# Kernel tuning notes

Measured on AMD Instinct MI355X. Metric: run time of the kernel, lower is better.

The kernel has to match this reference:

```python
import jax, jax.numpy as jnp
import numpy as np

D = 4
KERNEL = (3, 3, 3, 3)
CIN = 8
COUT = 16
SPATIAL = (24, 24, 24, 24)
B = 8


def setup_inputs() -> dict:
    key = jax.random.key(0)
    k1, k2, k3 = jax.random.split(key, 3)
    x = jax.random.normal(k1, (B, CIN) + SPATIAL, dtype=jnp.float32)
    kmul = int(np.prod(KERNEL))  # 81
    # torch layout: zeros(O, kmul, 1).repeat(1,1,Cin).reshape(O, kmul*Cin)
    # -> flat dim is kernel-major, channel-minor
    weight = jax.random.normal(k2, (COUT, kmul * CIN), dtype=jnp.float32) * 0.05
    bias = jax.random.normal(k3, (COUT,), dtype=jnp.float32) * 0.05
    return {"x": x, "weight": weight, "bias": bias}


def reference(x, weight, bias):
    # Unflatten weight to (O, k1, k2, k3, k4, Cin) matching the unfold's
    # (kernel..., channel) flatten order, then run a direct 4-D 'same' conv
    # (cross-correlation, identical math to the unfold+matmul original).
    w = weight.reshape((COUT,) + KERNEL + (CIN,))
    dn = jax.lax.ConvDimensionNumbers(
        lhs_spec=(0, 1, 2, 3, 4, 5),   # N, C, s1..s4
        rhs_spec=(0, 5, 1, 2, 3, 4),   # O, I, k1..k4  (I lives at axis 5 of w)
        out_spec=(0, 1, 2, 3, 4, 5),   # N, O, s1..s4
    )
    out = jax.lax.conv_general_dilated(
        x, w,
        window_strides=(1,) * D,
        padding=[(1, 1)] * D,
        dimension_numbers=dn,
    )
    return out + bias.reshape((1, COUT) + (1,) * D)
```

## Files before the change

### kernel.cpp

```cpp
#include <hip/hip_runtime.h>
#include <hip/hip_bf16.h>


#define SDIM  24
#define SP    (SDIM * SDIM * SDIM * SDIM)
#define CIN   8
#define COUT  16
#define BATCH 8
#define KW    648
#define NCHUNK 21
#define NB    4
#define PTILES (SP / 16)
#define NBLOCKS ((BATCH / NB) * PTILES / 4)
#define NXCD  8
#define CPX   (NBLOCKS / NXCD)

#define ZERO_OFF 0
#define WPK_OFF  256
#define XT_OFF   32768
#define XT_BYTES ((size_t)BATCH * SP * CIN * 2)
#define WS_NEEDED (XT_OFF + XT_BYTES)

typedef __attribute__((ext_vector_type(8))) short short8;
typedef __attribute__((ext_vector_type(4))) float f32x4;

static __device__ __forceinline__ unsigned short f2bf(float f) {
    unsigned u = __builtin_bit_cast(unsigned, f);
    u = (u + 0x7fffu + ((u >> 16) & 1u)) >> 16;
    return (unsigned short)u;
}

__global__ __launch_bounds__(256) void pack_weights(
    const float* __restrict__ w, unsigned char* __restrict__ ws)
{
    int t = blockIdx.x * 256 + threadIdx.x;
    if (t == 1344) {
        short8 z = {0,0,0,0,0,0,0,0};
        *(short8*)(ws + ZERO_OFF) = z;
    }
    if (t >= NCHUNK * 64) return;
    int chunk = t >> 6;
    int lane  = t & 63;
    int m     = lane & 15;
    int quad  = lane >> 4;
    short8 pk;
    #pragma unroll
    for (int j = 0; j < 8; ++j) {
        int k = chunk * 32 + quad * 8 + j;
        float f = (k < KW) ? w[m * KW + k] : 0.0f;
        pk[j] = (short)f2bf(f);
    }
    ((short8*)(ws + WPK_OFF))[chunk * 64 + lane] = pk;
}

__global__ __launch_bounds__(256) void transpose_x(
    const float* __restrict__ x, unsigned char* __restrict__ ws)
{
    int idx = blockIdx.x * 256 + threadIdx.x;
    int b  = idx / (SP / 2);
    int pp = idx - b * (SP / 2);
    int p  = pp * 2;
    const float* xb = x + (size_t)b * CIN * SP + p;

    float2 v[CIN];
    #pragma unroll
    for (int c = 0; c < CIN; ++c)
        v[c] = *(const float2*)(xb + (size_t)c * SP);

    union { __hip_bfloat162 h2[4]; short8 s8; } u0, u1;
    #pragma unroll
    for (int i = 0; i < 4; ++i) {
        float2 a = make_float2(v[2 * i].x, v[2 * i + 1].x);
        float2 bq = make_float2(v[2 * i].y, v[2 * i + 1].y);
        u0.h2[i] = __float22bfloat162_rn(a);
        u1.h2[i] = __float22bfloat162_rn(bq);
    }
    short8* dst = (short8*)(ws + XT_OFF) + ((size_t)b * SP + p);
    dst[0] = u0.s8;
    dst[1] = u1.s8;
}

__global__ __launch_bounds__(256) void conv4d_mfma(
    const unsigned char* __restrict__ ws,
    const float* __restrict__ bias,
    float* __restrict__ out)
{
    const int lane = threadIdx.x & 63;
    const int wave = threadIdx.x >> 6;
    const int col  = lane & 15;
    const int quad = lane >> 4;

    int bid = blockIdx.x;
    bid = (bid & (NXCD - 1)) * CPX + (bid >> 3);

    int W = bid * 4 + wave;
    W = __builtin_amdgcn_readfirstlane(W);
    const int pt = W % PTILES;
    const int g  = W / PTILES;

    const int p = pt * 16 + col;
    int r = p;
    const int p4 = r % SDIM; r /= SDIM;
    const int p3 = r % SDIM; r /= SDIM;
    const int p2 = r % SDIM;
    const int p1 = r / SDIM;

    const short8* wpk  = (const short8*)(ws + WPK_OFF);
    const short8* xT   = (const short8*)(ws + XT_OFF);
    const short8* zslt = (const short8*)(ws + ZERO_OFF);

    const short8* xb[NB];
    #pragma unroll
    for (int t = 0; t < NB; ++t)
        xb[t] = xT + (size_t)(g * NB + t) * SP;

    f32x4 acc[NB];
    #pragma unroll
    for (int t = 0; t < NB; ++t) acc[t] = (f32x4){0.f, 0.f, 0.f, 0.f};

    #pragma unroll
    for (int c = 0; c < NCHUNK; ++c) {
        short8 afrag = wpk[c * 64 + lane];

        int tap = c * 4 + quad;
        int k1 = tap / 27; int rem = tap - k1 * 27;
        int k2 = rem / 9;  rem -= k2 * 9;
        int k3 = rem / 3;
        int k4 = rem - k3 * 3;
        int q1 = p1 + k1 - 1, q2 = p2 + k2 - 1, q3 = p3 + k3 - 1, q4 = p4 + k4 - 1;
        bool valid = ((unsigned)q1 < (unsigned)SDIM) & ((unsigned)q2 < (unsigned)SDIM) &
                     ((unsigned)q3 < (unsigned)SDIM) & ((unsigned)q4 < (unsigned)SDIM);
        int q = ((q1 * SDIM + q2) * SDIM + q3) * SDIM + q4;

        short8 bf[NB];
        #pragma unroll
        for (int t = 0; t < NB; ++t) {
            const short8* src = valid ? (xb[t] + q) : zslt;
            bf[t] = *src;
        }
        #pragma unroll
        for (int t = 0; t < NB; ++t)
            acc[t] = __builtin_amdgcn_mfma_f32_16x16x32_bf16(afrag, bf[t], acc[t], 0, 0, 0);
    }

    f32x4 b4 = *(const f32x4*)(bias + quad * 4);
    #pragma unroll
    for (int t = 0; t < NB; ++t) {
        float* obase = out + ((size_t)(g * NB + t) * COUT + quad * 4) * SP + p;
        #pragma unroll
        for (int reg = 0; reg < 4; ++reg)
            obase[(size_t)reg * SP] = acc[t][reg] + b4[reg];
    }
}

__global__ __launch_bounds__(256) void conv4d_direct(
    const float* __restrict__ x, const float* __restrict__ w,
    const float* __restrict__ bias, float* __restrict__ out)
{
    int t = blockIdx.x * blockDim.x + threadIdx.x;
    int b = t / SP;
    int p = t - b * SP;
    int p4 = p % SDIM; int tmp = p / SDIM;
    int p3 = tmp % SDIM; tmp /= SDIM;
    int p2 = tmp % SDIM; int p1 = tmp / SDIM;
    float acc[COUT];
    #pragma unroll
    for (int o = 0; o < COUT; ++o) acc[o] = bias[o];
    const float* xb = x + (size_t)b * CIN * SP;
    for (int k1 = 0; k1 < 3; ++k1) {
        unsigned q1 = (unsigned)(p1 + k1 - 1); if (q1 >= SDIM) continue;
        for (int k2 = 0; k2 < 3; ++k2) {
            unsigned q2 = (unsigned)(p2 + k2 - 1); if (q2 >= SDIM) continue;
            for (int k3 = 0; k3 < 3; ++k3) {
                unsigned q3 = (unsigned)(p3 + k3 - 1); if (q3 >= SDIM) continue;
                int base123 = (((int)q1 * SDIM + (int)q2) * SDIM + (int)q3) * SDIM;
                int kf = ((k1 * 3 + k2) * 3 + k3) * 3;
                for (int k4 = 0; k4 < 3; ++k4) {
                    unsigned q4 = (unsigned)(p4 + k4 - 1); if (q4 >= SDIM) continue;
                    int q = base123 + (int)q4;
                    float xv[CIN];
                    #pragma unroll
                    for (int c = 0; c < CIN; ++c) xv[c] = xb[c * SP + q];
                    const float* wp = w + (kf + k4) * CIN;
                    #pragma unroll
                    for (int o = 0; o < COUT; ++o)
                        #pragma unroll
                        for (int c = 0; c < CIN; ++c)
                            acc[o] = fmaf(xv[c], wp[o * KW + c], acc[o]);
                }
            }
        }
    }
    float* ob = out + (size_t)b * COUT * SP + p;
    #pragma unroll
    for (int o = 0; o < COUT; ++o) ob[o * SP] = acc[o];
}

extern "C" void kernel_launch(void* const* d_in, const int* in_sizes, int n_in,
                              void* d_out, int out_size, void* d_ws, size_t ws_size,
                              hipStream_t stream)
{
    const float* x    = (const float*)d_in[0];
    const float* w    = (const float*)d_in[1];
    const float* bias = (const float*)d_in[2];
    float* out        = (float*)d_out;

    if (ws_size < WS_NEEDED) {
        const int total = BATCH * SP;
        hipLaunchKernelGGL(conv4d_direct, dim3(total / 256), dim3(256), 0, stream,
                           x, w, bias, out);
        return;
    }

    unsigned char* ws = (unsigned char*)d_ws;

    hipLaunchKernelGGL(pack_weights, dim3(6), dim3(256), 0, stream, w, ws);

    const int pair_total = BATCH * SP / 2;
    hipLaunchKernelGGL(transpose_x, dim3(pair_total / 256), dim3(256), 0, stream, x, ws);

    hipLaunchKernelGGL(conv4d_mfma, dim3(NBLOCKS), dim3(256), 0, stream,
                       (const unsigned char*)ws, bias, out);
}
```

Measured before the change: 366.8 us.

## Use zero-padded bf16 input layout to remove boundary checks in conv

```diff
diff --git a/kernel.cpp b/kernel.cpp
--- a/kernel.cpp
+++ b/kernel.cpp
@@ -4,6 +4,8 @@
 
 #define SDIM  24
 #define SP    (SDIM * SDIM * SDIM * SDIM)
+#define PD    26
+#define SPPAD (PD * PD * PD * PD)
 #define CIN   8
 #define COUT  16
 #define BATCH 8
@@ -12,14 +14,17 @@
 #define NB    4
 #define PTILES (SP / 16)
 #define NBLOCKS ((BATCH / NB) * PTILES / 4)
-#define NXCD  8
-#define CPX   (NBLOCKS / NXCD)
 
 #define ZERO_OFF 0
 #define WPK_OFF  256
 #define XT_OFF   32768
-#define XT_BYTES ((size_t)BATCH * SP * CIN * 2)
-#define WS_NEEDED (XT_OFF + XT_BYTES)
+#define XT_BYTES  ((size_t)BATCH * SP * CIN * 2)
+#define XTP_BYTES ((size_t)BATCH * SPPAD * CIN * 2)
+#define WS_NEEDED_OLD (XT_OFF + XT_BYTES)
+#define WS_NEEDED_PAD (XT_OFF + XTP_BYTES)
+
+#define ZTOTAL ((size_t)BATCH * SPPAD)
+#define ZBLOCKS 14281
 
 typedef __attribute__((ext_vector_type(8))) short short8;
 typedef __attribute__((ext_vector_type(4))) float f32x4;
@@ -30,14 +35,18 @@
     return (unsigned short)u;
 }
 
-__global__ __launch_bounds__(256) void pack_weights(
+__global__ __launch_bounds__(256) void prep0_pad(
     const float* __restrict__ w, unsigned char* __restrict__ ws)
 {
-    int t = blockIdx.x * 256 + threadIdx.x;
-    if (t == 1344) {
-        short8 z = {0,0,0,0,0,0,0,0};
-        *(short8*)(ws + ZERO_OFF) = z;
-    }
+    if (blockIdx.x < ZBLOCKS) {
+        size_t i = (size_t)blockIdx.x * 256 + threadIdx.x;
+        if (i < ZTOTAL) {
+            short8 z = {0, 0, 0, 0, 0, 0, 0, 0};
+            ((short8*)(ws + XT_OFF))[i] = z;
+        }
+        return;
+    }
+    int t = (blockIdx.x - ZBLOCKS) * 256 + threadIdx.x;
     if (t >= NCHUNK * 64) return;
     int chunk = t >> 6;
     int lane  = t & 63;
@@ -53,6 +62,138 @@
     ((short8*)(ws + WPK_OFF))[chunk * 64 + lane] = pk;
 }
 
+__global__ __launch_bounds__(256) void transpose_xp(
+    const float* __restrict__ x, unsigned char* __restrict__ ws)
+{
+    int idx = blockIdx.x * 256 + threadIdx.x;
+    int b  = idx / (SP / 4);
+    int pq = idx - b * (SP / 4);
+    int p  = pq * 4;
+    const float* xb = x + (size_t)b * CIN * SP + p;
+
+    float4 v[CIN];
+    #pragma unroll
+    for (int c = 0; c < CIN; ++c)
+        v[c] = *(const float4*)(xb + (size_t)c * SP);
+
+    union { __hip_bfloat162 h2[4]; short8 s8; } u[4];
+    #pragma unroll
+    for (int j = 0; j < 4; ++j) {
+        #pragma unroll
+        for (int i = 0; i < 4; ++i) {
+            float a0 = (&v[2 * i].x)[j];
+            float a1 = (&v[2 * i + 1].x)[j];
+            u[j].h2[i] = __float22bfloat162_rn(make_float2(a0, a1));
+        }
+    }
+
+    int r = p;
+    const int p4 = r % SDIM; r /= SDIM;
+    const int p3 = r % SDIM; r /= SDIM;
+    const int p2 = r % SDIM;
+    const int p1 = r / SDIM;
+    int qp = (((p1 + 1) * PD + (p2 + 1)) * PD + (p3 + 1)) * PD + (p4 + 1);
+
+    short8* dst = (short8*)(ws + XT_OFF) + (size_t)b * SPPAD + qp;
+    #pragma unroll
+    for (int j = 0; j < 4; ++j) dst[j] = u[j].s8;
+}
+
+__global__ __launch_bounds__(256) void conv4d_mfma_pad(
+    const unsigned char* __restrict__ ws,
+    const float* __restrict__ bias,
+    float* __restrict__ out)
+{
+    __shared__ int    s_delta[96];
+    __shared__ short8 s_w[NCHUNK * 64];
+
+    const int tid  = threadIdx.x;
+    const int lane = tid & 63;
+    const int wave = tid >> 6;
+    const int col  = lane & 15;
+    const int quad = lane >> 4;
+
+    const short8* wpk = (const short8*)(ws + WPK_OFF);
+    for (int t = tid; t < NCHUNK * 64; t += 256) s_w[t] = wpk[t];
+    if (tid < 84) {
+        int k1 = tid / 27, rem = tid - k1 * 27;
+        int k2 = rem / 9;  rem -= k2 * 9;
+        int k3 = rem / 3;
+        int k4 = rem - k3 * 3;
+        s_delta[tid] = (k1 * (PD * PD * PD) + k2 * (PD * PD) + k3 * PD + k4) * 16;
+    }
+    __syncthreads();
+
+    int W = blockIdx.x * 4 + wave;
+    W = __builtin_amdgcn_readfirstlane(W);
+    const int pt = W % PTILES;
+    const int g  = W / PTILES;
+
+    const int p = pt * 16 + col;
+    int r = p;
+    const int p4 = r % SDIM; r /= SDIM;
+    const int p3 = r % SDIM; r /= SDIM;
+    const int p2 = r % SDIM;
+    const int p1 = r / SDIM;
+    const int pidx16 = (((p1 * PD + p2) * PD + p3) * PD + p4) * 16;
+
+    const unsigned char* xbase[NB];
+    #pragma unroll
+    for (int t = 0; t < NB; ++t)
+        xbase[t] = ws + XT_OFF + (size_t)(g * NB + t) * SPPAD * 16;
+
+    f32x4 acc[NB];
+    #pragma unroll
+    for (int t = 0; t < NB; ++t) acc[t] = (f32x4){0.f, 0.f, 0.f, 0.f};
+
+    #pragma unroll
+    for (int c = 0; c < NCHUNK; ++c) {
+        short8 afrag = s_w[c * 64 + lane];
+        int voff = pidx16 + s_delta[c * 4 + quad];
+
+        short8 bf[NB];
+        #pragma unroll
+        for (int t = 0; t < NB; ++t)
+            bf[t] = *(const short8*)(xbase[t] + voff);
+        #pragma unroll
+        for (int t = 0; t < NB; ++t)
+            acc[t] = __builtin_amdgcn_mfma_f32_16x16x32_bf16(afrag, bf[t], acc[t], 0, 0, 0);
+    }
+
+    f32x4 b4 = *(const f32x4*)(bias + quad * 4);
+    #pragma unroll
+    for (int t = 0; t < NB; ++t) {
+        float* obase = out + ((size_t)(g * NB + t) * COUT + quad * 4) * SP + p;
+        #pragma unroll
+        for (int reg = 0; reg < 4; ++reg)
+            obase[(size_t)reg * SP] = acc[t][reg] + b4[reg];
+    }
+}
+
+
+__global__ __launch_bounds__(256) void pack_weights(
+    const float* __restrict__ w, unsigned char* __restrict__ ws)
+{
+    int t = blockIdx.x * 256 + threadIdx.x;
+    if (t == 1344) {
+        short8 z = {0,0,0,0,0,0,0,0};
+        *(short8*)(ws + ZERO_OFF) = z;
+    }
+    if (t >= NCHUNK * 64) return;
+    int chunk = t >> 6;
+    int lane  = t & 63;
+    int m     = lane & 15;
+    int quad  = lane >> 4;
+    short8 pk;
+    #pragma unroll
+    for (int j = 0; j < 8; ++j) {
+        int k = chunk * 32 + quad * 8 + j;
+        float f = (k < KW) ? w[m * KW + k] : 0.0f;
+        pk[j] = (short)f2bf(f);
+    }
+    ((short8*)(ws + WPK_OFF))[chunk * 64 + lane] = pk;
+}
+
 __global__ __launch_bounds__(256) void transpose_x(
     const float* __restrict__ x, unsigned char* __restrict__ ws)
 {
@@ -90,10 +231,7 @@
     const int col  = lane & 15;
     const int quad = lane >> 4;
 
-    int bid = blockIdx.x;
-    bid = (bid & (NXCD - 1)) * CPX + (bid >> 3);
-
-    int W = bid * 4 + wave;
+    int W = blockIdx.x * 4 + wave;
     W = __builtin_amdgcn_readfirstlane(W);
     const int pt = W % PTILES;
     const int g  = W / PTILES;
@@ -204,21 +342,27 @@
     const float* w    = (const float*)d_in[1];
     const float* bias = (const float*)d_in[2];
     float* out        = (float*)d_out;
-
-    if (ws_size < WS_NEEDED) {
-        const int total = BATCH * SP;
-        hipLaunchKernelGGL(conv4d_direct, dim3(total / 256), dim3(256), 0, stream,
-                           x, w, bias, out);
+    unsigned char* ws = (unsigned char*)d_ws;
+
+    if (ws_size >= WS_NEEDED_PAD) {
+        hipLaunchKernelGGL(prep0_pad, dim3(ZBLOCKS + 6), dim3(256), 0, stream, w, ws);
+        hipLaunchKernelGGL(transpose_xp, dim3(BATCH * SP / 4 / 256), dim3(256), 0, stream,
+                           x, ws);
+        hipLaunchKernelGGL(conv4d_mfma_pad, dim3(NBLOCKS), dim3(256), 0, stream,
+                           (const unsigned char*)ws, bias, out);
         return;
     }
 
-    unsigned char* ws = (unsigned char*)d_ws;
-
-    hipLaunchKernelGGL(pack_weights, dim3(6), dim3(256), 0, stream, w, ws);
-
-    const int pair_total = BATCH * SP / 2;
-    hipLaunchKernelGGL(transpose_x, dim3(pair_total / 256), dim3(256), 0, stream, x, ws);
-
-    hipLaunchKernelGGL(conv4d_mfma, dim3(NBLOCKS), dim3(256), 0, stream,
-                       (const unsigned char*)ws, bias, out);
-}
+    if (ws_size >= WS_NEEDED_OLD) {
+        hipLaunchKernelGGL(pack_weights, dim3(6), dim3(256), 0, stream, w, ws);
+        const int pair_total = BATCH * SP / 2;
+        hipLaunchKernelGGL(transpose_x, dim3(pair_total / 256), dim3(256), 0, stream, x, ws);
+        hipLaunchKernelGGL(conv4d_mfma, dim3(NBLOCKS), dim3(256), 0, stream,
+                           (const unsigned char*)ws, bias, out);
+        return;
+    }
+
+    const int total = BATCH * SP;
+    hipLaunchKernelGGL(conv4d_direct, dim3(total / 256), dim3(256), 0, stream,
+                       x, w, bias, out);
+}
```

After: 350.3 us. -4.5%, faster.
